# Optimization experiments

Hardware: AMD Instinct MI355X
Metric: run time of the kernel (lower is better)

Reference implementation:

```python
import jax, jax.numpy as jnp
import numpy as np

N = 50000      # nodes
E = 800000     # edges (avg degree 16)
C_IN = 64
C_OUT = 64
H = 32         # hidden_nf (hard-coded in module)
L = 4          # egnn_clean.EGNN default n_layers


def _lin(key, fan_in, fan_out):
    s = 1.0 / np.sqrt(fan_in)
    kw, kb = jax.random.split(key)
    w = jax.random.uniform(kw, (fan_in, fan_out), jnp.float32, -s, s)
    b = jax.random.uniform(kb, (fan_out,), jnp.float32, -s, s)
    return w, b


def _stack(key, fan_in, fan_out):
    ws, bs = zip(*[_lin(jax.random.fold_in(key, l), fan_in, fan_out) for l in range(L)])
    return jnp.stack(ws), jnp.stack(bs)


def setup_inputs() -> dict:
    key = jax.random.key(0)
    k = jax.random.split(key, 16)
    inp = {
        'data': jax.random.normal(k[0], (N, C_IN), jnp.float32),
        'pos': jax.random.normal(k[1], (N, 2), jnp.float32),
        'edge_attr': jax.random.normal(k[2], (E, 1), jnp.float32),
        't': jnp.ones((1,), jnp.float32),
        'row': jax.random.randint(k[3], (E,), 0, N),
        'col': jax.random.randint(k[4], (E,), 0, N),
    }
    inp['emb_in_w'], inp['emb_in_b'] = _lin(k[5], C_IN + 1, H)
    inp['emb_out_w'], inp['emb_out_b'] = _lin(k[6], H, C_OUT)
    inp['edge_w1'], inp['edge_b1'] = _stack(k[7], 2 * H + 2, H)  # [h_i, h_j, radial, edge_attr]
    inp['edge_w2'], inp['edge_b2'] = _stack(k[8], H, H)
    inp['node_w1'], inp['node_b1'] = _stack(k[9], 2 * H, H)
    inp['node_w2'], inp['node_b2'] = _stack(k[10], H, H)
    inp['coord_w1'], inp['coord_b1'] = _stack(k[11], H, H)
    lim = 0.001 * np.sqrt(6.0 / (H + 1))  # xavier_uniform gain=0.001, no bias
    inp['coord_w2'] = jax.random.uniform(k[12], (L, H, 1), jnp.float32, -lim, lim)
    return inp


def _egnn(data, pos, edge_attr, t, emb_in_w, emb_in_b, edge_w1, edge_b1, edge_w2, edge_b2,
          node_w1, node_b1, node_w2, node_b2, coord_w1, coord_b1, coord_w2,
          emb_out_w, emb_out_b, row, col):
    n = data.shape[0]
    silu = jax.nn.silu
    # prepend time channel; pad 2D coords with a zero z-column
    h = jnp.concatenate([jnp.broadcast_to(t.reshape(1, 1), (n, 1)), data], axis=1)  # [N, C_IN+1]
    x = jnp.concatenate([pos, jnp.zeros((n, 1), pos.dtype)], axis=1)                # [N, 3]
    h = h @ emb_in_w + emb_in_b                                                     # [N, H]
    ones_e = jnp.ones((row.shape[0], 1), x.dtype)
    cnt = jnp.maximum(jax.ops.segment_sum(ones_e, row, num_segments=n), 1.0)        # [N,1] clamp(min=1)
    for l in range(L):
        diff = x[row] - x[col]                                    # [E, 3]
        radial = jnp.sum(diff * diff, axis=1, keepdims=True)      # [E, 1]
        ein = jnp.concatenate([h[row], h[col], radial, edge_attr], axis=1)  # [E, 2H+2]
        m = silu(silu(ein @ edge_w1[l] + edge_b1[l]) @ edge_w2[l] + edge_b2[l])  # edge MLP [E, H]
        # equivariant coordinate update (coords_agg='mean')
        phi = silu(m @ coord_w1[l] + coord_b1[l]) @ coord_w2[l]   # [E, 1]
        x = x + jax.ops.segment_sum(diff * phi, row, num_segments=n) / cnt
        # node update (sum aggregation, residual)
        agg = jax.ops.segment_sum(m, row, num_segments=n)         # [N, H]
        upd = silu(jnp.concatenate([h, agg], axis=1) @ node_w1[l] + node_b1[l]) @ node_w2[l] + node_b2[l]
        h = h + upd
    return h @ emb_out_w + emb_out_b                              # [N, C_OUT]


def reference(data, pos, edge_attr, t, emb_in_w, emb_in_b, edge_w1, edge_b1, edge_w2, edge_b2,
              node_w1, node_b1, node_w2, node_b2, coord_w1, coord_b1, coord_w2,
              emb_out_w, emb_out_b, row, col):
    return _egnn(data, pos, edge_attr, t, emb_in_w, emb_in_b, edge_w1, edge_b1, edge_w2, edge_b2,
                 node_w1, node_b1, node_w2, node_b2, coord_w1, coord_b1, coord_w2,
                 emb_out_w, emb_out_b, row, col)
```

## Files before the change

kernel.cpp:

```cpp
#include <hip/hip_runtime.h>
#include <hip/hip_fp16.h>

#define NN 50000
#define NE 800000
#define CIN 64
#define COUT 64
#define HD 32
#define NL 4
#define NB_SCAN 49

typedef float f32x4 __attribute__((ext_vector_type(4)));
typedef _Float16 half8 __attribute__((ext_vector_type(8)));

__device__ __forceinline__ float silu_f(float v) {
    return v * __builtin_amdgcn_rcpf(1.0f + __expf(-v));
}

__global__ __launch_bounds__(256) void embed_kernel(
    const float* __restrict__ data, const float* __restrict__ pos,
    const float* __restrict__ tptr,
    const float* __restrict__ W, const float* __restrict__ b,
    const float* __restrict__ eW1_0,
    float* __restrict__ h, float* __restrict__ x4,
    float* __restrict__ Hr, float* __restrict__ Hc,
    int* __restrict__ cursor, float* __restrict__ aggM, float* __restrict__ aggX4)
{
    int n = blockIdx.x * 256 + threadIdx.x;
    if (n >= NN) return;
    float t = tptr[0];
    float d[CIN];
    const float4* dp = (const float4*)(data + (size_t)n * CIN);
#pragma unroll
    for (int i = 0; i < CIN / 4; i++) {
        float4 v = dp[i];
        d[4*i+0] = v.x; d[4*i+1] = v.y; d[4*i+2] = v.z; d[4*i+3] = v.w;
    }
    float acc[HD];
#pragma unroll
    for (int j = 0; j < HD; j++) acc[j] = fmaf(t, W[j], b[j]);
#pragma unroll
    for (int i = 0; i < CIN; i++) {
        float a = d[i];
#pragma unroll
        for (int j = 0; j < HD; j++) acc[j] = fmaf(a, W[(i + 1) * HD + j], acc[j]);
    }
    float4* hp = (float4*)(h + (size_t)n * HD);
#pragma unroll
    for (int j = 0; j < HD / 4; j++)
        hp[j] = make_float4(acc[4*j], acc[4*j+1], acc[4*j+2], acc[4*j+3]);
    ((float4*)x4)[n] = make_float4(pos[n*2+0], pos[n*2+1], 0.0f, 0.0f);

    float a1[HD], a2[HD];
#pragma unroll
    for (int j = 0; j < HD; j++) { a1[j] = 0.0f; a2[j] = 0.0f; }
#pragma unroll
    for (int i = 0; i < HD; i++) {
        float z = acc[i];
#pragma unroll
        for (int j = 0; j < HD; j++) {
            a1[j] = fmaf(z, eW1_0[i * HD + j], a1[j]);
            a2[j] = fmaf(z, eW1_0[(HD + i) * HD + j], a2[j]);
        }
    }
    float4* rp = (float4*)(Hr + (size_t)n * HD);
    float4* cp = (float4*)(Hc + (size_t)n * HD);
#pragma unroll
    for (int j = 0; j < HD/4; j++) {
        rp[j] = make_float4(a1[4*j], a1[4*j+1], a1[4*j+2], a1[4*j+3]);
        cp[j] = make_float4(a2[4*j], a2[4*j+1], a2[4*j+2], a2[4*j+3]);
    }

    cursor[n] = 0;
    float4 z4 = make_float4(0.f, 0.f, 0.f, 0.f);
    float4* za = (float4*)(aggM + (size_t)n * HD);
#pragma unroll
    for (int j = 0; j < HD/4; j++) za[j] = z4;
    ((float4*)aggX4)[n] = z4;
}

__global__ __launch_bounds__(128) void prep_kernel(
    const float* __restrict__ eW2, const float* __restrict__ cW1,
    __half* __restrict__ w2B, __half* __restrict__ cW1B)
{
    int l  = blockIdx.x;
    int nt = threadIdx.x >> 6;
    int wl = threadIdx.x & 63;
    int rsel = wl & 15, ksel = wl >> 4;
#pragma unroll
    for (int e = 0; e < 8; e++) {
        int k = 8 * ksel + e;
        int j = 16 * nt + rsel;
        size_t o = ((size_t)(l * 2 + nt) * 64 + wl) * 8 + e;
        w2B[o]  = __float2half(eW2[(size_t)l * HD * HD + k * HD + j]);
        cW1B[o] = __float2half(cW1[(size_t)l * HD * HD + k * HD + j]);
    }
}

__global__ __launch_bounds__(256) void hist_kernel(const int* __restrict__ row,
                                                   int* __restrict__ cnt)
{
    int e = blockIdx.x * 256 + threadIdx.x;
    if (e < NE) atomicAdd(&cnt[row[e]], 1);
}

__global__ __launch_bounds__(1024) void scanA_kernel(const int* __restrict__ cnt,
                                                     int* __restrict__ rowstart,
                                                     int* __restrict__ bsum)
{
    __shared__ int sd[1024];
    int i = blockIdx.x * 1024 + threadIdx.x;
    int v = (i < NN) ? cnt[i] : 0;
    sd[threadIdx.x] = v;
    __syncthreads();
    for (int off = 1; off < 1024; off <<= 1) {
        int t = (threadIdx.x >= (unsigned)off) ? sd[threadIdx.x - off] : 0;
        __syncthreads();
        sd[threadIdx.x] += t;
        __syncthreads();
    }
    if (i < NN) rowstart[i] = sd[threadIdx.x] - v;
    if (threadIdx.x == 1023) bsum[blockIdx.x] = sd[1023];
}

__global__ __launch_bounds__(1024) void scanC_kernel(int* __restrict__ rowstart,
                                                     const int* __restrict__ bsum,
                                                     int* __restrict__ cursor)
{
    __shared__ int sb[64];
    if (threadIdx.x < 64) {
        int lane = threadIdx.x;
        int v = (lane < NB_SCAN) ? bsum[lane] : 0;
        int x = v;
        for (int off = 1; off < 64; off <<= 1) {
            int y = __shfl_up(x, off);
            if (lane >= off) x += y;
        }
        sb[lane] = x - v;
        if (lane == 63) rowstart[NN] = x;
    }
    __syncthreads();
    int i = blockIdx.x * 1024 + threadIdx.x;
    if (i < NN) {
        rowstart[i] += sb[blockIdx.x];
        cursor[i] = 0;
    }
}

__global__ __launch_bounds__(256) void scatter_kernel(
    const int* __restrict__ row, const int* __restrict__ col,
    const float* __restrict__ edge_attr,
    const int* __restrict__ rowstart, int* __restrict__ cursor,
    int* __restrict__ srow, int* __restrict__ scol, float* __restrict__ sea)
{
    int e = blockIdx.x * 256 + threadIdx.x;
    if (e >= NE) return;
    int r = row[e];
    int p = rowstart[r] + atomicAdd(&cursor[r], 1);
    srow[p] = r;
    scol[p] = col[e];
    sea[p]  = edge_attr[e];
}

__global__ __launch_bounds__(256) void edge_fused_kernel(
    const float* __restrict__ x4,
    const int* __restrict__ srow, const int* __restrict__ scol,
    const float* __restrict__ sea,
    const float* __restrict__ Hr, const float* __restrict__ Hc,
    const float* __restrict__ eW1, const float* __restrict__ eb1,
    const float* __restrict__ eb2,
    const __half* __restrict__ w2Bl, const __half* __restrict__ cW1Bl,
    const float* __restrict__ cb1, const float* __restrict__ cW2,
    const int* __restrict__ rowstart,
    float* __restrict__ aggM, float* __restrict__ aggX4)
{
    __shared__ __align__(16) __half At[256][40];
    __shared__ __half sx[256][4];
    __shared__ float  phib[256];
    __shared__ int snf, snl;
    int tid = threadIdx.x;
    int s_base = blockIdx.x * 256;
    int s = s_base + tid;
    int r = srow[s], c = scol[s];
    if (tid == 0)   snf = r;
    if (tid == 255) snl = r;

    float4 xr = ((const float4*)x4)[r];
    float4 xc = ((const float4*)x4)[c];
    float d0 = xr.x - xc.x, d1 = xr.y - xc.y, d2 = xr.z - xc.z;
    float radial = d0*d0 + d1*d1 + d2*d2;
    float ea = sea[s];

    const f32x4* hrp = (const f32x4*)(Hr + (size_t)r * HD);
    const f32x4* hcp = (const f32x4*)(Hc + (size_t)c * HD);
    const f32x4* w64 = (const f32x4*)(eW1 + 64 * HD);
    const f32x4* w65 = (const f32x4*)(eW1 + 65 * HD);
    const f32x4* bb1 = (const f32x4*)eb1;
    int wbuf[16];
#pragma unroll
    for (int i = 0; i < 8; i++) {
        f32x4 v = hrp[i] + hcp[i] + bb1[i] + radial * w64[i] + ea * w65[i];
        v.x = silu_f(v.x); v.y = silu_f(v.y); v.z = silu_f(v.z); v.w = silu_f(v.w);
        __half2 p0 = __floats2half2_rn(v.x, v.y);
        __half2 p1 = __floats2half2_rn(v.z, v.w);
        wbuf[2*i]   = *(int*)&p0;
        wbuf[2*i+1] = *(int*)&p1;
    }
    int4* arow = (int4*)&At[tid][0];
#pragma unroll
    for (int q = 0; q < 4; q++)
        arow[q] = make_int4(wbuf[4*q], wbuf[4*q+1], wbuf[4*q+2], wbuf[4*q+3]);

    int wl = tid & 63;
    int wbase = tid & 192;
    int rsel = wl & 15, ksel = wl >> 4;

    half8 bw0 = ((const half8*)w2Bl)[wl];
    half8 bw1 = ((const half8*)w2Bl)[64 + wl];
    float bc0 = eb2[rsel], bc1 = eb2[16 + rsel];
    f32x4 acc[4][2];
#pragma unroll
    for (int mt = 0; mt < 4; mt++) {
        acc[mt][0] = (f32x4){bc0, bc0, bc0, bc0};
        acc[mt][1] = (f32x4){bc1, bc1, bc1, bc1};
    }
#pragma unroll
    for (int mt = 0; mt < 4; mt++) {
        half8 af = *(const half8*)&At[wbase + 16*mt + rsel][8*ksel];
        acc[mt][0] = __builtin_amdgcn_mfma_f32_16x16x32_f16(af, bw0, acc[mt][0], 0, 0, 0);
        acc[mt][1] = __builtin_amdgcn_mfma_f32_16x16x32_f16(af, bw1, acc[mt][1], 0, 0, 0);
    }
#pragma unroll
    for (int mt = 0; mt < 4; mt++)
#pragma unroll
        for (int nt = 0; nt < 2; nt++)
#pragma unroll
            for (int q = 0; q < 4; q++) {
                float mv = silu_f(acc[mt][nt][q]);
                At[wbase + 16*mt + 4*ksel + q][16*nt + rsel] = __float2half(mv);
            }

    half8 cw0 = ((const half8*)cW1Bl)[wl];
    half8 cw1 = ((const half8*)cW1Bl)[64 + wl];
    float cc0 = cb1[rsel], cc1 = cb1[16 + rsel];
    f32x4 cacc[4][2];
#pragma unroll
    for (int mt = 0; mt < 4; mt++) {
        cacc[mt][0] = (f32x4){cc0, cc0, cc0, cc0};
        cacc[mt][1] = (f32x4){cc1, cc1, cc1, cc1};
    }
#pragma unroll
    for (int mt = 0; mt < 4; mt++) {
        half8 am = *(const half8*)&At[wbase + 16*mt + rsel][8*ksel];
        cacc[mt][0] = __builtin_amdgcn_mfma_f32_16x16x32_f16(am, cw0, cacc[mt][0], 0, 0, 0);
        cacc[mt][1] = __builtin_amdgcn_mfma_f32_16x16x32_f16(am, cw1, cacc[mt][1], 0, 0, 0);
    }

    float cw2a = cW2[rsel], cw2b = cW2[16 + rsel];
    float p[4][4];
#pragma unroll
    for (int mt = 0; mt < 4; mt++)
#pragma unroll
        for (int q = 0; q < 4; q++)
            p[mt][q] = silu_f(cacc[mt][0][q]) * cw2a + silu_f(cacc[mt][1][q]) * cw2b;
#pragma unroll
    for (int dd = 1; dd < 16; dd <<= 1)
#pragma unroll
        for (int mt = 0; mt < 4; mt++)
#pragma unroll
            for (int q = 0; q < 4; q++)
                p[mt][q] += __shfl_xor(p[mt][q], dd);
    if (rsel == 0) {
#pragma unroll
        for (int mt = 0; mt < 4; mt++)
#pragma unroll
            for (int q = 0; q < 4; q++)
                phib[wbase + 16*mt + 4*ksel + q] = p[mt][q];
    }
    float phi = phib[tid];

    *(__half2*)&sx[tid][0] = __floats2half2_rn(d0 * phi, d1 * phi);
    sx[tid][2] = __float2half(d2 * phi);
    __syncthreads();

    int g = tid >> 5, ch = tid & 31;
    int nf = snf, nl = snl;
    for (int node = nf + g; node <= nl; node += 8) {
        int lo = rowstart[node], hi = rowstart[node + 1];
        int clo = lo - s_base; if (clo < 0) clo = 0;
        int chi = hi - s_base; if (chi > 256) chi = 256;
        if (chi <= clo) continue;
        float am = 0.0f;
        for (int j = clo; j < chi; j++) am += __half2float(At[j][ch]);
        bool interior = (lo >= s_base) && (hi <= s_base + 256);
        if (interior) aggM[(size_t)node * HD + ch] = am;
        else          atomicAdd(&aggM[(size_t)node * HD + ch], am);
        if (ch < 3) {
            float ax = 0.0f;
            for (int j = clo; j < chi; j++) ax += __half2float(sx[j][ch]);
            if (interior) aggX4[(size_t)node * 4 + ch] = ax;
            else          atomicAdd(&aggX4[(size_t)node * 4 + ch], ax);
        }
    }
}

__global__ __launch_bounds__(256) void node_fused_kernel(
    float* __restrict__ h, float* __restrict__ x4,
    float* __restrict__ aggM, float* __restrict__ aggX4,
    const int* __restrict__ rowstart,
    const float* __restrict__ nW1, const float* __restrict__ nb1,
    const float* __restrict__ nW2, const float* __restrict__ nb2,
    const float* __restrict__ eW1n,
    float* __restrict__ Hr, float* __restrict__ Hc,
    const float* __restrict__ Wout, const float* __restrict__ bout,
    float* __restrict__ out)
{
    __shared__ float sIn[8][2*HD];
    __shared__ float sU[8][HD];
    __shared__ float sH[8][HD];
    int local = threadIdx.x >> 5;
    int ch    = threadIdx.x & 31;
    int n = blockIdx.x * 8 + local;
    float hv = h[(size_t)n * HD + ch];
    float am = aggM[(size_t)n * HD + ch];
    aggM[(size_t)n * HD + ch] = 0.0f;
    sIn[local][ch]      = hv;
    sIn[local][HD + ch] = am;
    if (ch < 3) {
        int cnt = rowstart[n + 1] - rowstart[n];
        float cf = (cnt < 1) ? 1.0f : (float)cnt;
        x4[(size_t)n * 4 + ch] += aggX4[(size_t)n * 4 + ch] / cf;
        aggX4[(size_t)n * 4 + ch] = 0.0f;
    }
    __syncthreads();
    float u1 = nb1[ch];
#pragma unroll 8
    for (int i = 0; i < 2*HD; i++) u1 = fmaf(sIn[local][i], nW1[i * HD + ch], u1);
    u1 = silu_f(u1);
    sU[local][ch] = u1;
    __syncthreads();
    float u2 = nb2[ch];
#pragma unroll 8
    for (int i = 0; i < HD; i++) u2 = fmaf(sU[local][i], nW2[i * HD + ch], u2);
    float hn = hv + u2;

    if (eW1n != nullptr) {
        h[(size_t)n * HD + ch] = hn;
        sH[local][ch] = hn;
        __syncthreads();
        float a = 0.0f, b = 0.0f;
#pragma unroll 8
        for (int i = 0; i < HD; i++) {
            float z = sH[local][i];
            a = fmaf(z, eW1n[i * HD + ch], a);
            b = fmaf(z, eW1n[(HD + i) * HD + ch], b);
        }
        Hr[(size_t)n * HD + ch] = a;
        Hc[(size_t)n * HD + ch] = b;
    } else {
        sH[local][ch] = hn;
        __syncthreads();
        float o0 = bout[ch], o1 = bout[HD + ch];
#pragma unroll 8
        for (int i = 0; i < HD; i++) {
            float z = sH[local][i];
            o0 = fmaf(z, Wout[i * COUT + ch], o0);
            o1 = fmaf(z, Wout[i * COUT + HD + ch], o1);
        }
        out[(size_t)n * COUT + ch]      = o0;
        out[(size_t)n * COUT + HD + ch] = o1;
    }
}

extern "C" void kernel_launch(void* const* d_in, const int* in_sizes, int n_in,
                              void* d_out, int out_size, void* d_ws, size_t ws_size,
                              hipStream_t stream) {
    const float* data      = (const float*)d_in[0];
    const float* pos       = (const float*)d_in[1];
    const float* edge_attr = (const float*)d_in[2];
    const float* tptr      = (const float*)d_in[3];
    const int*   row       = (const int*)d_in[4];
    const int*   col       = (const int*)d_in[5];
    const float* emb_in_w  = (const float*)d_in[6];
    const float* emb_in_b  = (const float*)d_in[7];
    const float* emb_out_w = (const float*)d_in[8];
    const float* emb_out_b = (const float*)d_in[9];
    const float* edge_w1   = (const float*)d_in[10];
    const float* edge_b1   = (const float*)d_in[11];
    const float* edge_w2   = (const float*)d_in[12];
    const float* edge_b2   = (const float*)d_in[13];
    const float* node_w1   = (const float*)d_in[14];
    const float* node_b1   = (const float*)d_in[15];
    const float* node_w2   = (const float*)d_in[16];
    const float* node_b2   = (const float*)d_in[17];
    const float* coord_w1  = (const float*)d_in[18];
    const float* coord_b1  = (const float*)d_in[19];
    const float* coord_w2  = (const float*)d_in[20];
    float* out = (float*)d_out;

    float* ws = (float*)d_ws;
    float* h      = ws;
    float* x4     = ws + 1600000;
    float* Hr     = ws + 1800000;
    float* Hc     = ws + 3400000;
    float* sea    = ws + 5000000;
    float* aggM   = ws + 5800000;
    float* aggX4  = ws + 7400000;
    int* rowstart = (int*)(ws + 7600000);
    int* cursor   = (int*)(ws + 7650004);
    int* srow     = (int*)(ws + 7700004);
    int* scol     = (int*)(ws + 8500004);
    int* bsum     = (int*)(ws + 9300004);
    __half* w2B   = (__half*)(ws + 9310000);
    __half* cW1B  = w2B + (size_t)NL * 1024;

    embed_kernel<<<(NN + 255) / 256, 256, 0, stream>>>(
        data, pos, tptr, emb_in_w, emb_in_b, edge_w1 ,
        h, x4, Hr, Hc, cursor, aggM, aggX4);
    prep_kernel<<<NL, 128, 0, stream>>>(edge_w2, coord_w1, w2B, cW1B);
    hist_kernel<<<NE / 256, 256, 0, stream>>>(row, cursor);
    scanA_kernel<<<NB_SCAN, 1024, 0, stream>>>(cursor, rowstart, bsum);
    scanC_kernel<<<NB_SCAN, 1024, 0, stream>>>(rowstart, bsum, cursor);
    scatter_kernel<<<NE / 256, 256, 0, stream>>>(row, col, edge_attr, rowstart, cursor, srow, scol, sea);

    for (int l = 0; l < NL; l++) {
        edge_fused_kernel<<<NE / 256, 256, 0, stream>>>(
            x4, srow, scol, sea, Hr, Hc,
            edge_w1 + l * (2*HD+2) * HD, edge_b1 + l * HD,
            edge_b2 + l * HD,
            w2B + (size_t)l * 1024, cW1B + (size_t)l * 1024,
            coord_b1 + l * HD, coord_w2 + l * HD,
            rowstart, aggM, aggX4);
        bool lastl = (l + 1 == NL);
        node_fused_kernel<<<NN / 8, 256, 0, stream>>>(
            h, x4, aggM, aggX4, rowstart,
            node_w1 + l * 2 * HD * HD, node_b1 + l * HD,
            node_w2 + l * HD * HD,     node_b2 + l * HD,
            lastl ? nullptr : (edge_w1 + (l + 1) * (2*HD+2) * HD), Hr, Hc,
            emb_out_w, emb_out_b, lastl ? out : nullptr);
    }
}
```

Measured before the change: 470.9 us.

## Store precomputed node projections in fp16 and pack sorted edge records

The per-node projections Hr/Hc used by the edge MLP are now stored as fp16 instead of fp32, which halves the bytes gathered per edge for the random row and column lookups. The sorted edge arrays (row, col, edge_attr) are packed into one int4 record per edge, so each edge needs a single 16-byte load instead of three separate loads. The fp16 storage and fp16 addition lower the precision of the first edge-layer pre-activation, and the workspace layout is reshuffled to fit the new buffers.

```diff
diff --git a/kernel.cpp b/kernel.cpp
--- a/kernel.cpp
+++ b/kernel.cpp
@@ -22,7 +22,7 @@
     const float* __restrict__ W, const float* __restrict__ b,
     const float* __restrict__ eW1_0,
     float* __restrict__ h, float* __restrict__ x4,
-    float* __restrict__ Hr, float* __restrict__ Hc,
+    __half* __restrict__ Hrh, __half* __restrict__ Hch,
     int* __restrict__ cursor, float* __restrict__ aggM, float* __restrict__ aggX4)
 {
     int n = blockIdx.x * 256 + threadIdx.x;
@@ -62,12 +62,20 @@
             a2[j] = fmaf(z, eW1_0[(HD + i) * HD + j], a2[j]);
         }
     }
-    float4* rp = (float4*)(Hr + (size_t)n * HD);
-    float4* cp = (float4*)(Hc + (size_t)n * HD);
-#pragma unroll
-    for (int j = 0; j < HD/4; j++) {
-        rp[j] = make_float4(a1[4*j], a1[4*j+1], a1[4*j+2], a1[4*j+3]);
-        cp[j] = make_float4(a2[4*j], a2[4*j+1], a2[4*j+2], a2[4*j+3]);
+    int w1[16], w2[16];
+#pragma unroll
+    for (int q = 0; q < 16; q++) {
+        __half2 p1 = __floats2half2_rn(a1[2*q], a1[2*q+1]);
+        __half2 p2 = __floats2half2_rn(a2[2*q], a2[2*q+1]);
+        w1[q] = *(int*)&p1;
+        w2[q] = *(int*)&p2;
+    }
+    int4* rp = (int4*)(Hrh + (size_t)n * HD);
+    int4* cp = (int4*)(Hch + (size_t)n * HD);
+#pragma unroll
+    for (int q = 0; q < 4; q++) {
+        rp[q] = make_int4(w1[4*q], w1[4*q+1], w1[4*q+2], w1[4*q+3]);
+        cp[q] = make_int4(w2[4*q], w2[4*q+1], w2[4*q+2], w2[4*q+3]);
     }
 
     cursor[n] = 0;
@@ -150,22 +158,19 @@
     const int* __restrict__ row, const int* __restrict__ col,
     const float* __restrict__ edge_attr,
     const int* __restrict__ rowstart, int* __restrict__ cursor,
-    int* __restrict__ srow, int* __restrict__ scol, float* __restrict__ sea)
+    int4* __restrict__ sedge)
 {
     int e = blockIdx.x * 256 + threadIdx.x;
     if (e >= NE) return;
     int r = row[e];
     int p = rowstart[r] + atomicAdd(&cursor[r], 1);
-    srow[p] = r;
-    scol[p] = col[e];
-    sea[p]  = edge_attr[e];
+    sedge[p] = make_int4(r, col[e], __float_as_int(edge_attr[e]), 0);
 }
 
 __global__ __launch_bounds__(256) void edge_fused_kernel(
     const float* __restrict__ x4,
-    const int* __restrict__ srow, const int* __restrict__ scol,
-    const float* __restrict__ sea,
-    const float* __restrict__ Hr, const float* __restrict__ Hc,
+    const int4* __restrict__ sedge,
+    const __half* __restrict__ Hrh, const __half* __restrict__ Hch,
     const float* __restrict__ eW1, const float* __restrict__ eb1,
     const float* __restrict__ eb2,
     const __half* __restrict__ w2Bl, const __half* __restrict__ cW1Bl,
@@ -180,7 +185,9 @@
     int tid = threadIdx.x;
     int s_base = blockIdx.x * 256;
     int s = s_base + tid;
-    int r = srow[s], c = scol[s];
+    int4 ei = sedge[s];
+    int r = ei.x, c = ei.y;
+    float ea = __int_as_float(ei.z);
     if (tid == 0)   snf = r;
     if (tid == 255) snl = r;
 
@@ -188,22 +195,21 @@
     float4 xc = ((const float4*)x4)[c];
     float d0 = xr.x - xc.x, d1 = xr.y - xc.y, d2 = xr.z - xc.z;
     float radial = d0*d0 + d1*d1 + d2*d2;
-    float ea = sea[s];
-
-    const f32x4* hrp = (const f32x4*)(Hr + (size_t)r * HD);
-    const f32x4* hcp = (const f32x4*)(Hc + (size_t)c * HD);
-    const f32x4* w64 = (const f32x4*)(eW1 + 64 * HD);
-    const f32x4* w65 = (const f32x4*)(eW1 + 65 * HD);
-    const f32x4* bb1 = (const f32x4*)eb1;
+
+    const half8* hr8 = (const half8*)(Hrh + (size_t)r * HD);
+    const half8* hc8 = (const half8*)(Hch + (size_t)c * HD);
     int wbuf[16];
 #pragma unroll
-    for (int i = 0; i < 8; i++) {
-        f32x4 v = hrp[i] + hcp[i] + bb1[i] + radial * w64[i] + ea * w65[i];
-        v.x = silu_f(v.x); v.y = silu_f(v.y); v.z = silu_f(v.z); v.w = silu_f(v.w);
-        __half2 p0 = __floats2half2_rn(v.x, v.y);
-        __half2 p1 = __floats2half2_rn(v.z, v.w);
-        wbuf[2*i]   = *(int*)&p0;
-        wbuf[2*i+1] = *(int*)&p1;
+    for (int i = 0; i < 4; i++) {
+        half8 s8 = hr8[i] + hc8[i];
+#pragma unroll
+        for (int k = 0; k < 8; k += 2) {
+            int j = 8*i + k;
+            float v0 = (float)s8[k]   + eb1[j]   + radial * eW1[64*HD+j]   + ea * eW1[65*HD+j];
+            float v1 = (float)s8[k+1] + eb1[j+1] + radial * eW1[64*HD+j+1] + ea * eW1[65*HD+j+1];
+            __half2 p = __floats2half2_rn(silu_f(v0), silu_f(v1));
+            wbuf[(j >> 1)] = *(int*)&p;
+        }
     }
     int4* arow = (int4*)&At[tid][0];
 #pragma unroll
@@ -310,7 +316,7 @@
     const float* __restrict__ nW1, const float* __restrict__ nb1,
     const float* __restrict__ nW2, const float* __restrict__ nb2,
     const float* __restrict__ eW1n,
-    float* __restrict__ Hr, float* __restrict__ Hc,
+    __half* __restrict__ Hrh, __half* __restrict__ Hch,
     const float* __restrict__ Wout, const float* __restrict__ bout,
     float* __restrict__ out)
 {
@@ -354,8 +360,8 @@
             a = fmaf(z, eW1n[i * HD + ch], a);
             b = fmaf(z, eW1n[(HD + i) * HD + ch], b);
         }
-        Hr[(size_t)n * HD + ch] = a;
-        Hc[(size_t)n * HD + ch] = b;
+        Hrh[(size_t)n * HD + ch] = __float2half(a);
+        Hch[(size_t)n * HD + ch] = __float2half(b);
     } else {
         sH[local][ch] = hn;
         __syncthreads();
@@ -400,31 +406,29 @@
     float* ws = (float*)d_ws;
     float* h      = ws;
     float* x4     = ws + 1600000;
-    float* Hr     = ws + 1800000;
-    float* Hc     = ws + 3400000;
-    float* sea    = ws + 5000000;
-    float* aggM   = ws + 5800000;
-    float* aggX4  = ws + 7400000;
-    int* rowstart = (int*)(ws + 7600000);
-    int* cursor   = (int*)(ws + 7650004);
-    int* srow     = (int*)(ws + 7700004);
-    int* scol     = (int*)(ws + 8500004);
-    int* bsum     = (int*)(ws + 9300004);
-    __half* w2B   = (__half*)(ws + 9310000);
+    __half* Hrh   = (__half*)(ws + 1800000);
+    __half* Hch   = (__half*)(ws + 2600000);
+    float* aggM   = ws + 3400000;
+    float* aggX4  = ws + 5000000;
+    int* rowstart = (int*)(ws + 5200000);
+    int* cursor   = (int*)(ws + 5250004);
+    int4* sedge   = (int4*)(ws + 5400000);
+    int* bsum     = (int*)(ws + 8600000);
+    __half* w2B   = (__half*)(ws + 8600100);
     __half* cW1B  = w2B + (size_t)NL * 1024;
 
     embed_kernel<<<(NN + 255) / 256, 256, 0, stream>>>(
         data, pos, tptr, emb_in_w, emb_in_b, edge_w1 ,
-        h, x4, Hr, Hc, cursor, aggM, aggX4);
+        h, x4, Hrh, Hch, cursor, aggM, aggX4);
     prep_kernel<<<NL, 128, 0, stream>>>(edge_w2, coord_w1, w2B, cW1B);
     hist_kernel<<<NE / 256, 256, 0, stream>>>(row, cursor);
     scanA_kernel<<<NB_SCAN, 1024, 0, stream>>>(cursor, rowstart, bsum);
     scanC_kernel<<<NB_SCAN, 1024, 0, stream>>>(rowstart, bsum, cursor);
-    scatter_kernel<<<NE / 256, 256, 0, stream>>>(row, col, edge_attr, rowstart, cursor, srow, scol, sea);
+    scatter_kernel<<<NE / 256, 256, 0, stream>>>(row, col, edge_attr, rowstart, cursor, sedge);
 
     for (int l = 0; l < NL; l++) {
         edge_fused_kernel<<<NE / 256, 256, 0, stream>>>(
-            x4, srow, scol, sea, Hr, Hc,
+            x4, sedge, Hrh, Hch,
             edge_w1 + l * (2*HD+2) * HD, edge_b1 + l * HD,
             edge_b2 + l * HD,
             w2B + (size_t)l * 1024, cW1B + (size_t)l * 1024,
@@ -435,7 +439,7 @@
             h, x4, aggM, aggX4, rowstart,
             node_w1 + l * 2 * HD * HD, node_b1 + l * HD,
             node_w2 + l * HD * HD,     node_b2 + l * HD,
-            lastl ? nullptr : (edge_w1 + (l + 1) * (2*HD+2) * HD), Hr, Hc,
+            lastl ? nullptr : (edge_w1 + (l + 1) * (2*HD+2) * HD), Hrh, Hch,
             emb_out_w, emb_out_b, lastl ? out : nullptr);
     }
 }
```

After: 458.9 us. -2.5%, faster.
